# Kernel tuning notes

Measured on AMD Instinct MI355X. Metric: run time of the kernel, lower is better.

The kernel has to match this reference:

```python
import jax, jax.numpy as jnp
import numpy as np

B, L, D, H = 4, 1024, 1024, 16
E = 16384
HD = D // H  # head dim = 64


def setup_inputs() -> dict:
    key = jax.random.key(0)
    k1, k2, k3, k4 = jax.random.split(key, 4)
    x = jax.random.normal(k1, (B, L, D), dtype=jnp.float32)
    edges = jax.random.randint(k2, (E, 2), 0, L, dtype=jnp.int32)
    w_qkv = jax.random.normal(k3, (3 * D, D), dtype=jnp.float32) * 0.02
    b_qkv = jnp.zeros((3 * D,), dtype=jnp.float32)
    w_out = jax.random.normal(k4, (D, D), dtype=jnp.float32) * 0.02
    b_out = jnp.zeros((D,), dtype=jnp.float32)
    return {"x": x, "edges": edges, "w_qkv": w_qkv, "b_qkv": b_qkv,
            "w_out": w_out, "b_out": b_out}


def reference(x, edges, w_qkv, b_qkv, w_out, b_out):
    # Build symmetric boolean adjacency mask [L, L]; True = edge present.
    adj = jnp.zeros((L, L), dtype=bool)
    adj = adj.at[edges[:, 0], edges[:, 1]].set(True)
    adj = adj.at[edges[:, 1], edges[:, 0]].set(True)

    # Fused QKV projection (torch MultiheadAttention in_proj).
    qkv = x @ w_qkv.T + b_qkv                      # [B, L, 3D]
    q, k, v = jnp.split(qkv, 3, axis=-1)           # each [B, L, D]

    def heads(t):  # [B, L, D] -> [B, H, L, HD]
        return t.reshape(B, L, H, HD).transpose(0, 2, 1, 3)

    q, k, v = heads(q), heads(k), heads(v)
    scale = 1.0 / np.sqrt(HD)
    scores = jnp.einsum('bhqd,bhkd->bhqk', q * scale, k)  # [B, H, L, L]
    # torch bool attn_mask: True means NOT allowed to attend -> -inf.
    scores = jnp.where(adj[None, None, :, :], -jnp.inf, scores)
    attn = jax.nn.softmax(scores, axis=-1)
    out = jnp.einsum('bhqk,bhkd->bhqd', attn, v)   # [B, H, L, HD]
    out = out.transpose(0, 2, 1, 3).reshape(B, L, D)
    return out @ w_out.T + b_out
```

## Files before the change

### kernel.cpp

```cpp
#include <hip/hip_runtime.h>
#include <hip/hip_bf16.h>
#include <stdint.h>

#define B_   4
#define L_   1024
#define D_   1024
#define H_   16
#define HD_  64
#define E_   16384
#define BH_  (B_*H_)
#define BL_  (B_*L_)

typedef __bf16 bf16;
typedef __bf16 bf16x8 __attribute__((ext_vector_type(8)));
typedef float  f32x4  __attribute__((ext_vector_type(4)));
typedef unsigned short u16x8 __attribute__((ext_vector_type(8)));

#if __has_builtin(__builtin_amdgcn_exp2f)
#define EXP2F(x) __builtin_amdgcn_exp2f(x)
#else
#define EXP2F(x) exp2f(x)
#endif

#define QSCALE 0.18033688011112042f

__device__ __forceinline__ void gload_lds16(const bf16* gsrc, bf16* lds_dst) {
  __builtin_amdgcn_global_load_lds(
      (const __attribute__((address_space(1))) unsigned int*)gsrc,
      (__attribute__((address_space(3))) unsigned int*)lds_dst,
      16, 0, 0);
}

__global__ __launch_bounds__(256) void k_castall(
    const void* __restrict__ x, const void* __restrict__ wq,
    const void* __restrict__ wo, const void* __restrict__ bq,
    const void* __restrict__ bo,
    const int* __restrict__ edges, unsigned long long* __restrict__ adj,
    bf16* __restrict__ xb, bf16* __restrict__ wqb, bf16* __restrict__ wob,
    float* __restrict__ bqf, float* __restrict__ bof,
    unsigned int* __restrict__ flag_out) {
  const int t = threadIdx.x;

  bool lf = false;
  {
    u16x8 u = *(const u16x8*)((const unsigned short*)wq + (size_t)t * 8);
#pragma unroll
    for (int q = 0; q < 8; ++q) lf |= (((u[q] >> 7) & 0xFF) >= 200);
  }
  const bool f = __any(lf);
  if (blockIdx.x == 0 && t == 0 && f) *flag_out = 1u;

  if (blockIdx.x < 64) {
    int i = blockIdx.x * 256 + t;
    int a = edges[2 * i], b = edges[2 * i + 1];
    atomicOr(&adj[a * 16 + (b >> 6)], 1ull << (b & 63));
    atomicOr(&adj[b * 16 + (a >> 6)], 1ull << (a & 63));
  }

  const long e = ((long)blockIdx.x * 256 + t) * 8;
  const long N0 = 4l << 20, N1 = N0 + (3l << 20), N2 = N1 + (1l << 20);
  const void* src;
  bf16* d16 = nullptr; float* d32 = nullptr; long j;
  if (e < N0)      { src = x;  d16 = xb;  j = e; }
  else if (e < N1) { src = wq; d16 = wqb; j = e - N0; }
  else if (e < N2) { src = wo; d16 = wob; j = e - N1; }
  else {
    long b = e - N2;
    if (b < 3072)      { src = bq; d32 = bqf; j = b; }
    else if (b < 4096) { src = bo; d32 = bof; j = b - 3072; }
    else return;
  }
  if (d16) {
    bf16x8 v;
    if (f) {
      const float* s = (const float*)src + j;
#pragma unroll
      for (int q = 0; q < 8; ++q) v[q] = (bf16)s[q];
    } else {
      v = *(const bf16x8*)((const bf16*)src + j);
    }
    *(bf16x8*)(d16 + j) = v;
  } else {
    if (f) {
      const f32x4* s = (const f32x4*)((const float*)src + j);
      f32x4 a = s[0], b2 = s[1];
      *(f32x4*)(d32 + j) = a;
      *((f32x4*)(d32 + j) + 1) = b2;
    } else {
      const bf16* s = (const bf16*)src + j;
#pragma unroll
      for (int q = 0; q < 8; ++q) d32[j + q] = (float)s[q];
    }
  }
}

template <bool QKV>
__global__ __launch_bounds__(512, 4) void k_gemm(
    const bf16* __restrict__ A, const bf16* __restrict__ W,
    const float* __restrict__ bias, void* __restrict__ outv,
    const unsigned int* __restrict__ flag,
    bf16* __restrict__ qb, bf16* __restrict__ kb, bf16* __restrict__ vb) {
  constexpr int K = 1024;
  __shared__ __align__(16) bf16 As[2 * 128 * 32];
  __shared__ __align__(16) bf16 Bs[2 * 128 * 32];

  const int t = threadIdx.x;
  const int lane = t & 63, w = t >> 6;
  const int wm = w >> 1, wn = w & 1;
  const int quad = lane >> 4, l16 = lane & 15;
  const int m0 = blockIdx.y * 128, n0 = blockIdx.x * 128;

  const bf16* Abase = A + m0 * K;
  const bf16* Wbase = W + n0 * K;

  const int srow = t >> 2;
  const int scol = (((t & 3) << 4) ^ (((srow >> 1) & 3) << 4)) >> 1;
  const bf16* asrc = Abase + srow * K + scol;
  const bf16* wsrc = Wbase + srow * K + scol;

  const int fo = ((quad * 16) ^ (((l16 >> 1) & 3) << 4)) >> 1;

  f32x4 acc[2][4] = {};

#define STAGE_AB(it1) do {                                 \
    const int bo_ = ((it1) & 1) * 4096;                    \
    gload_lds16(asrc + (it1) * 32, &As[bo_ + w * 512]);    \
    gload_lds16(wsrc + (it1) * 32, &Bs[bo_ + w * 512]);    \
  } while (0)

  STAGE_AB(0);

#pragma unroll 1
  for (int it = 0; it < 32; ++it) {
    const int bo = (it & 1) * 4096;

    if (it < 31) STAGE_AB(it + 1);

    if (it < 31) asm volatile("s_waitcnt vmcnt(2)" ::: "memory");
    else         asm volatile("s_waitcnt vmcnt(0)" ::: "memory");
    __builtin_amdgcn_s_barrier();

    bf16x8 af[2], bfv[4];
#pragma unroll
    for (int i = 0; i < 2; ++i)
      af[i] = *(const bf16x8*)&As[bo + (wm * 32 + i * 16 + l16) * 32 + fo];
#pragma unroll
    for (int j = 0; j < 4; ++j)
      bfv[j] = *(const bf16x8*)&Bs[bo + (wn * 64 + j * 16 + l16) * 32 + fo];
#pragma unroll
    for (int mi = 0; mi < 2; ++mi)
#pragma unroll
      for (int ni = 0; ni < 4; ++ni)
        acc[mi][ni] = __builtin_amdgcn_mfma_f32_16x16x32_bf16(
            af[mi], bfv[ni], acc[mi][ni], 0, 0, 0);
    __builtin_amdgcn_s_barrier();
  }
#undef STAGE_AB

#pragma unroll
  for (int ni = 0; ni < 4; ++ni) {
    int col = n0 + wn * 64 + ni * 16 + l16;
    float bv = bias[col];
    if constexpr (QKV) {
      int which = col >> 10;
      int hcol = col & 1023;
      int h = hcol >> 6, hd = hcol & 63;
#pragma unroll
      for (int mi = 0; mi < 2; ++mi)
#pragma unroll
        for (int r = 0; r < 4; ++r) {
          int row = m0 + wm * 32 + mi * 16 + quad * 4 + r;
          int bb = row >> 10, l = row & 1023;
          int bh = bb * H_ + h;
          float v = acc[mi][ni][r] + bv;
          if (which == 0)      qb[(bh * L_ + l) * HD_ + hd] = (bf16)(v * QSCALE);
      else if (which == 1)     kb[(bh * L_ + l) * HD_ + hd] = (bf16)v;
      else                     vb[(bh * HD_ + hd) * L_ + l] = (bf16)v;
        }
    } else {
      bool f32out = (*flag != 0);
#pragma unroll
      for (int mi = 0; mi < 2; ++mi)
#pragma unroll
        for (int r = 0; r < 4; ++r) {
          int row = m0 + wm * 32 + mi * 16 + quad * 4 + r;
          float v = acc[mi][ni][r] + bv;
          if (f32out) ((float*)outv)[row * 1024 + col] = v;
          else        ((bf16*)outv)[row * 1024 + col] = (bf16)v;
        }
    }
  }
}

__global__ __launch_bounds__(256, 4) void k_attn(
    const bf16* __restrict__ qb, const bf16* __restrict__ kb,
    const bf16* __restrict__ vb, const unsigned long long* __restrict__ adj,
    bf16* __restrict__ aout) {
  __shared__ __align__(16) bf16 Ks[2 * 64 * 64];
  __shared__ __align__(16) bf16 Vt[2 * 64 * 64];
  __shared__ __align__(16) bf16 Ps[64 * 64];

  const int t = threadIdx.x, lane = t & 63, w = t >> 6;
  const int quad = lane >> 4, l16 = lane & 15;
  const int bh = blockIdx.y, qt = blockIdx.x;
  const int q0 = qt * 64 + w * 16;

  const bf16* qbase = qb + (size_t)bh * (L_ * HD_);
  const bf16* kbase = kb + (size_t)bh * (L_ * HD_);
  const bf16* vbase = vb + (size_t)bh * (HD_ * L_);

  bf16x8 aq[2];
#pragma unroll
  for (int c = 0; c < 2; ++c)
    aq[c] = *(const bf16x8*)&qbase[(q0 + l16) * HD_ + c * 32 + quad * 8];

  const int vr = lane >> 3;
  const int scol = ((lane & 7) ^ vr) * 8;
  const bf16* ksrc0 = kbase + (w * 16 + vr) * HD_ + scol;
  const bf16* ksrc1 = kbase + (w * 16 + 8 + vr) * HD_ + scol;
  const bf16* vsrc0 = vbase + (w * 16 + vr) * L_ + scol;
  const bf16* vsrc1 = vbase + (w * 16 + 8 + vr) * L_ + scol;

  const unsigned long long* adjrow = adj + (size_t)(q0 + quad * 4) * 16;

  float l_acc[4] = {0.f, 0.f, 0.f, 0.f};
  f32x4 o_acc[4] = {};

  const int psoff = (quad * 16) ^ ((l16 & 7) << 4);
  const int pswrow = (w * 16 + quad * 4) * 64;

#define STAGE_KV(i1) do {                                          \
    const int bo_ = ((i1) & 1) * 4096;                             \
    gload_lds16(ksrc0 + (i1) * 4096, &Ks[bo_ + (w * 16) * 64]);     \
    gload_lds16(ksrc1 + (i1) * 4096, &Ks[bo_ + (w * 16 + 8) * 64]); \
    gload_lds16(vsrc0 + (i1) * 64,   &Vt[bo_ + (w * 16) * 64]);     \
    gload_lds16(vsrc1 + (i1) * 64,   &Vt[bo_ + (w * 16 + 8) * 64]); \
  } while (0)

  STAGE_KV(0);

#pragma unroll 1
  for (int i = 0; i < 16; ++i) {
    const int bufo = (i & 1) * 4096;

    unsigned long long wmask[4];
#pragma unroll
    for (int r = 0; r < 4; ++r) wmask[r] = adjrow[r * 16 + i];

    if (i < 15) STAGE_KV(i + 1);

    if (i < 15) asm volatile("s_waitcnt vmcnt(8)" ::: "memory");
    else        asm volatile("s_waitcnt vmcnt(4)" ::: "memory");
    __builtin_amdgcn_s_barrier();

    f32x4 s[4];
#pragma unroll
    for (int nt = 0; nt < 4; ++nt) {
      f32x4 z = {};
#pragma unroll
      for (int c = 0; c < 2; ++c) {
        bf16x8 bk = *(const bf16x8*)&Ks[bufo + (nt * 16 + l16) * 64 +
            ((psoff ^ (c << 6)) >> 1)];
        z = __builtin_amdgcn_mfma_f32_16x16x32_bf16(aq[c], bk, z, 0, 0, 0);
      }
      s[nt] = z;
    }

#pragma unroll
    for (int r = 0; r < 4; ++r) {
      unsigned long long wr = wmask[r] >> l16;
      float pr = 0.f;
#pragma unroll
      for (int nt = 0; nt < 4; ++nt) {
        float sv = s[nt][r];
        if ((wr >> (nt * 16)) & 1ull) sv = -60000.f;
        float p = EXP2F(sv);
        int colb = (nt * 32 + l16 * 2) ^ (((quad * 4 + r) & 7) << 4);
        Ps[pswrow + r * 64 + (colb >> 1)] = (bf16)p;
        pr += p;
      }
      l_acc[r] += pr;
    }

#pragma unroll
    for (int c = 0; c < 2; ++c) {
      bf16x8 ap = *(const bf16x8*)
          &Ps[(w * 16 + l16) * 64 + ((psoff ^ (c << 6)) >> 1)];
#pragma unroll
      for (int nt = 0; nt < 4; ++nt) {
        bf16x8 bv = *(const bf16x8*)
            &Vt[bufo + (nt * 16 + l16) * 64 + ((psoff ^ (c << 6)) >> 1)];
        o_acc[nt] = __builtin_amdgcn_mfma_f32_16x16x32_bf16(ap, bv, o_acc[nt], 0, 0, 0);
      }
    }
    __builtin_amdgcn_s_barrier();
  }
#undef STAGE_KV

#pragma unroll
  for (int x = 1; x < 16; x <<= 1)
#pragma unroll
    for (int r = 0; r < 4; ++r)
      l_acc[r] += __shfl_xor(l_acc[r], x, 64);

  const int bb = bh >> 4, h = bh & 15;
#pragma unroll
  for (int r = 0; r < 4; ++r) {
    const float inv = l_acc[r] > 0.f ? 1.f / l_acc[r] : 0.f;
    const int qrow = q0 + quad * 4 + r;
    bf16* orow = aout + ((size_t)(bb * L_ + qrow)) * D_ + h * HD_;
#pragma unroll
    for (int nt = 0; nt < 4; ++nt)
      orow[nt * 16 + l16] = (bf16)(o_acc[nt][r] * inv);
  }
}

extern "C" void kernel_launch(void* const* d_in, const int* in_sizes, int n_in,
                              void* d_out, int out_size, void* d_ws, size_t ws_size,
                              hipStream_t stream) {
  const void* x_raw  = d_in[0];
  const int*  edges  = (const int*)d_in[1];
  const void* wq_raw = d_in[2];
  const void* bq_raw = d_in[3];
  const void* wo_raw = d_in[4];
  const void* bo_raw = d_in[5];

  char* ws = (char*)d_ws;
  unsigned int*        flag = (unsigned int*)ws;
  unsigned long long*  adj  = (unsigned long long*)(ws + 1024);
  size_t off = 1024 + 131072;
  bf16* xb    = (bf16*)(ws + off); off += (size_t)BL_ * D_ * 2;
  bf16* wqkvb = (bf16*)(ws + off); off += (size_t)3 * D_ * D_ * 2;
  bf16* woutb = (bf16*)(ws + off); off += (size_t)D_ * D_ * 2;
  float* bqf  = (float*)(ws + off); off += 3 * D_ * 4;
  float* bof  = (float*)(ws + off); off += D_ * 4;
  bf16* qb    = (bf16*)(ws + off); off += (size_t)BH_ * L_ * HD_ * 2;
  bf16* kb    = (bf16*)(ws + off); off += (size_t)BH_ * L_ * HD_ * 2;
  bf16* vb    = (bf16*)(ws + off); off += (size_t)BH_ * L_ * HD_ * 2;
  bf16* abuf  = (bf16*)(ws + off);

  hipMemsetAsync(ws, 0, 1024 + 131072, stream);

  k_castall<<<dim3(4098), dim3(256), 0, stream>>>(
      x_raw, wq_raw, wo_raw, bq_raw, bo_raw, edges, adj,
      xb, wqkvb, woutb, bqf, bof, flag);

  k_gemm<true><<<dim3(24, 32), dim3(512), 0, stream>>>(
      xb, wqkvb, bqf, nullptr, flag, qb, kb, vb);
  k_attn<<<dim3(16, 64), dim3(256), 0, stream>>>(qb, kb, vb, adj, abuf);
  k_gemm<false><<<dim3(8, 32), dim3(512), 0, stream>>>(
      abuf, woutb, bof, d_out, flag, nullptr, nullptr, nullptr);
}
```

Measured before the change: 189.0 us.

## Triple-buffer GEMM LDS tiles and prefetch register fragments ahead of MFMA

Moves the GEMM main loop from a double-buffered LDS scheme to a three-slot rotation, with two K-steps per loop iteration. Fragments for the next K-step are read from LDS into registers before the MFMAs for the current step issue, so LDS reads overlap matrix math. One barrier per K-step remains, but the trailing barrier is gone. The cost is 50% more shared memory and more live registers, which could reduce occupancy under launch_bounds(512,4), plus more complex buffer-index bookkeeping.

```diff
diff --git a/kernel.cpp b/kernel.cpp
--- a/kernel.cpp
+++ b/kernel.cpp
@@ -101,8 +101,8 @@
     const unsigned int* __restrict__ flag,
     bf16* __restrict__ qb, bf16* __restrict__ kb, bf16* __restrict__ vb) {
   constexpr int K = 1024;
-  __shared__ __align__(16) bf16 As[2 * 128 * 32];
-  __shared__ __align__(16) bf16 Bs[2 * 128 * 32];
+  __shared__ __align__(16) bf16 As[3 * 4096];
+  __shared__ __align__(16) bf16 Bs[3 * 4096];
 
   const int t = threadIdx.x;
   const int lane = t & 63, w = t >> 6;
@@ -122,40 +122,62 @@
 
   f32x4 acc[2][4] = {};
 
-#define STAGE_AB(it1) do {                                 \
-    const int bo_ = ((it1) & 1) * 4096;                    \
-    gload_lds16(asrc + (it1) * 32, &As[bo_ + w * 512]);    \
-    gload_lds16(wsrc + (it1) * 32, &Bs[bo_ + w * 512]);    \
-  } while (0)
-
-  STAGE_AB(0);
+  struct Frags { bf16x8 a0, a1, b0, b1, b2, b3; };
+  auto STAGE = [&](int kt, int lo) {
+    gload_lds16(asrc + kt * 32, &As[lo + w * 512]);
+    gload_lds16(wsrc + kt * 32, &Bs[lo + w * 512]);
+  };
+  auto RD = [&](int lo) {
+    Frags f;
+    f.a0 = *(const bf16x8*)&As[lo + (wm * 32 +  0 + l16) * 32 + fo];
+    f.a1 = *(const bf16x8*)&As[lo + (wm * 32 + 16 + l16) * 32 + fo];
+    f.b0 = *(const bf16x8*)&Bs[lo + (wn * 64 +  0 + l16) * 32 + fo];
+    f.b1 = *(const bf16x8*)&Bs[lo + (wn * 64 + 16 + l16) * 32 + fo];
+    f.b2 = *(const bf16x8*)&Bs[lo + (wn * 64 + 32 + l16) * 32 + fo];
+    f.b3 = *(const bf16x8*)&Bs[lo + (wn * 64 + 48 + l16) * 32 + fo];
+    return f;
+  };
+  auto MM = [&](const Frags& f) {
+    acc[0][0] = __builtin_amdgcn_mfma_f32_16x16x32_bf16(f.a0, f.b0, acc[0][0], 0, 0, 0);
+    acc[0][1] = __builtin_amdgcn_mfma_f32_16x16x32_bf16(f.a0, f.b1, acc[0][1], 0, 0, 0);
+    acc[0][2] = __builtin_amdgcn_mfma_f32_16x16x32_bf16(f.a0, f.b2, acc[0][2], 0, 0, 0);
+    acc[0][3] = __builtin_amdgcn_mfma_f32_16x16x32_bf16(f.a0, f.b3, acc[0][3], 0, 0, 0);
+    acc[1][0] = __builtin_amdgcn_mfma_f32_16x16x32_bf16(f.a1, f.b0, acc[1][0], 0, 0, 0);
+    acc[1][1] = __builtin_amdgcn_mfma_f32_16x16x32_bf16(f.a1, f.b1, acc[1][1], 0, 0, 0);
+    acc[1][2] = __builtin_amdgcn_mfma_f32_16x16x32_bf16(f.a1, f.b2, acc[1][2], 0, 0, 0);
+    acc[1][3] = __builtin_amdgcn_mfma_f32_16x16x32_bf16(f.a1, f.b3, acc[1][3], 0, 0, 0);
+  };
+
+  STAGE(0, 0);
+  STAGE(1, 4096);
+  asm volatile("s_waitcnt vmcnt(2)" ::: "memory");
+  __builtin_amdgcn_s_barrier();
+  Frags fA = RD(0);
+
+  int o0 = 0, o1 = 4096, o2 = 8192;
 
 #pragma unroll 1
-  for (int it = 0; it < 32; ++it) {
-    const int bo = (it & 1) * 4096;
-
-    if (it < 31) STAGE_AB(it + 1);
-
-    if (it < 31) asm volatile("s_waitcnt vmcnt(2)" ::: "memory");
-    else         asm volatile("s_waitcnt vmcnt(0)" ::: "memory");
+  for (int it = 0; it < 32; it += 2) {
+    if (it + 2 < 32) {
+      STAGE(it + 2, o2);
+      asm volatile("s_waitcnt vmcnt(2)" ::: "memory");
+    } else {
+      asm volatile("s_waitcnt vmcnt(0)" ::: "memory");
+    }
     __builtin_amdgcn_s_barrier();
-
-    bf16x8 af[2], bfv[4];
-#pragma unroll
-    for (int i = 0; i < 2; ++i)
-      af[i] = *(const bf16x8*)&As[bo + (wm * 32 + i * 16 + l16) * 32 + fo];
-#pragma unroll
-    for (int j = 0; j < 4; ++j)
-      bfv[j] = *(const bf16x8*)&Bs[bo + (wn * 64 + j * 16 + l16) * 32 + fo];
-#pragma unroll
-    for (int mi = 0; mi < 2; ++mi)
-#pragma unroll
-      for (int ni = 0; ni < 4; ++ni)
-        acc[mi][ni] = __builtin_amdgcn_mfma_f32_16x16x32_bf16(
-            af[mi], bfv[ni], acc[mi][ni], 0, 0, 0);
+    Frags fB = RD(o1);
+    MM(fA);
+    if (it + 3 < 32) {
+      STAGE(it + 3, o0);
+      asm volatile("s_waitcnt vmcnt(2)" ::: "memory");
+    } else {
+      asm volatile("s_waitcnt vmcnt(0)" ::: "memory");
+    }
     __builtin_amdgcn_s_barrier();
-  }
-#undef STAGE_AB
+    if (it + 2 < 32) fA = RD(o2);
+    MM(fB);
+    int tmp = o2; o2 = o1; o1 = o0; o0 = tmp;
+  }
 
 #pragma unroll
   for (int ni = 0; ni < 4; ++ni) {
```

Measured after the change: 198.3 us. 1.05x slower.
